# Performance work log

Measured on AMD Instinct MI355X. Metric: run time of the kernel, lower is better.

## Reference

```python
import jax, jax.numpy as jnp
import numpy as np

B, S, H = 2, 2048, 1024
N, DK = 16, 64          # heads, key/value dim (N*DK == H)
DF = 4096               # FFN hidden
SCALE = 1.0 / float(DK) ** 0.5
EPS = 1e-5


def _layer_norm(x, g, b):
    mu = jnp.mean(x, axis=-1, keepdims=True)
    var = jnp.var(x, axis=-1, keepdims=True)
    return (x - mu) * jax.lax.rsqrt(var + EPS) * g + b


def setup_inputs() -> dict:
    key = jax.random.key(0)
    ks = jax.random.split(key, 12)
    s = 0.02
    return {
        "x": jax.random.normal(ks[0], (B, S, H), dtype=jnp.float32),
        "Wq": jax.random.normal(ks[1], (N * DK, H), dtype=jnp.float32) * s,
        "bq": jnp.zeros((N * DK,), jnp.float32),
        "Wk": jax.random.normal(ks[2], (N * DK, H), dtype=jnp.float32) * s,
        "bk": jnp.zeros((N * DK,), jnp.float32),
        "Wv": jax.random.normal(ks[3], (N * DK, H), dtype=jnp.float32) * s,
        "bv": jnp.zeros((N * DK,), jnp.float32),
        "Wo": jax.random.normal(ks[4], (H, N * DK), dtype=jnp.float32) * s,
        "bo": jnp.zeros((H,), jnp.float32),
        "W1": jax.random.normal(ks[5], (DF, H), dtype=jnp.float32) * s,
        "b1": jnp.zeros((DF,), jnp.float32),
        "W2": jax.random.normal(ks[6], (H, DF), dtype=jnp.float32) * s,
        "b2": jnp.zeros((H,), jnp.float32),
        "ln1_g": jnp.ones((H,), jnp.float32),
        "ln1_b": jnp.zeros((H,), jnp.float32),
        "ln2_g": jnp.ones((H,), jnp.float32),
        "ln2_b": jnp.zeros((H,), jnp.float32),
    }


def _mha(x, Wq, bq, Wk, bk, Wv, bv, Wo, bo):
    b = x.shape[0]
    q = (x @ Wq.T + bq).reshape(b, -1, N, DK)  # [B,T,N,DK]
    k = (x @ Wk.T + bk).reshape(b, -1, N, DK)
    v = (x @ Wv.T + bv).reshape(b, -1, N, DK)
    # naive full-score attention, faithful to torch einsum layout
    scores = jnp.einsum('btnd,bsnd->tsbn', q, k) * SCALE  # [T,S,B,N]
    p = jax.nn.softmax(scores, axis=1)                    # softmax over S (dim=1)
    attn = jnp.einsum('tsbn,bsnd->btnd', p, v)            # [B,T,N,DK]
    attn = attn.reshape(b, attn.shape[1], -1)             # [B,T,N*DK]
    return attn @ Wo.T + bo


def reference(x, Wq, bq, Wk, bk, Wv, bv, Wo, bo, W1, b1, W2, b2,
              ln1_g, ln1_b, ln2_g, ln2_b):
    # post-LN encoder layer: x = LN(x + MHA(x)); x = LN(x + FFN(x))
    h = _layer_norm(x + _mha(x, Wq, bq, Wk, bk, Wv, bv, Wo, bo), ln1_g, ln1_b)
    ff = jax.nn.relu(h @ W1.T + b1) @ W2.T + b2
    return _layer_norm(h + ff, ln2_g, ln2_b)
```

## Files before the change

kernel.cpp:

```cpp
#include <hip/hip_runtime.h>
#include <stdint.h>


typedef unsigned short u16;
typedef __bf16 bf16x8 __attribute__((ext_vector_type(8)));
typedef float  f32x4  __attribute__((ext_vector_type(4)));

__device__ __forceinline__ u16 f2bf(float f) {
    unsigned int u = __float_as_uint(f);
    u += 0x7FFFu + ((u >> 16) & 1u);
    return (u16)(u >> 16);
}

__device__ __forceinline__ float bf2f(u16 v) {
    return __uint_as_float((unsigned)v << 16);
}

__device__ __forceinline__ unsigned pack_bf16_hi(float lo, float hi) {
#if __has_builtin(__builtin_amdgcn_perm)
    return __builtin_amdgcn_perm(__float_as_uint(hi), __float_as_uint(lo), 0x07060302u);
#else
    return (__float_as_uint(lo) >> 16) | (__float_as_uint(hi) & 0xFFFF0000u);
#endif
}

__device__ __forceinline__ void async_load16(const u16* g, u16* l) {
    __builtin_amdgcn_global_load_lds(
        (__attribute__((address_space(1))) void*)g,
        (__attribute__((address_space(3))) void*)l, 16, 0, 0);
}

struct CvtArgs {
    const float* src[7];
    u16*         dst[7];
    int          n[7];
};

__global__ __launch_bounds__(256) void k_cvt_all(CvtArgs a) {
    const int seg = blockIdx.y;
    const int i = (blockIdx.x * 256 + threadIdx.x) * 8;
    if (i >= a.n[seg]) return;
    const float* in = a.src[seg];
    u16* out = a.dst[seg];
    float4 x = *(const float4*)(in + i);
    float4 y = *(const float4*)(in + i + 4);
    uint4 o;
    o.x = (unsigned)f2bf(x.x) | ((unsigned)f2bf(x.y) << 16);
    o.y = (unsigned)f2bf(x.z) | ((unsigned)f2bf(x.w) << 16);
    o.z = (unsigned)f2bf(y.x) | ((unsigned)f2bf(y.y) << 16);
    o.w = (unsigned)f2bf(y.z) | ((unsigned)f2bf(y.w) << 16);
    *(uint4*)(out + i) = o;
}

__global__ __launch_bounds__(256) void k_concat3(const float* __restrict__ a,
                                                 const float* __restrict__ b,
                                                 const float* __restrict__ c,
                                                 float* __restrict__ out) {
    int i = blockIdx.x * 256 + threadIdx.x;
    if (i >= 3072) return;
    out[i] = (i < 1024) ? a[i] : (i < 2048 ? b[i - 1024] : c[i - 2048]);
}

template<int OUT_BF16, int RELU>
__global__ __launch_bounds__(256, 4) void k_gemm_bt(
    const u16* __restrict__ A, const u16* __restrict__ Bw,
    const float* __restrict__ bias, void* __restrict__ Y,
    int M, int N, int K)
{
    __shared__ u16 As[128 * 32];
    __shared__ u16 Bs[128 * 32];
    const int tid  = threadIdx.x;
    const int wave = tid >> 6, lane = tid & 63;
    const int lm = lane & 15, lq = lane >> 4;
    const int m0 = blockIdx.x * 128, n0 = blockIdx.y * 128;
    const int wr = (wave >> 1) * 64, wc = (wave & 1) * 64;

    const int ksz = K / gridDim.z;
    const int ks  = blockIdx.z * ksz, ke = ks + ksz;

    const size_t arow = (size_t)(m0 + (lane >> 2)) * K + (lane & 3) * 8;
    const size_t brow = (size_t)(n0 + (lane >> 2)) * K + (lane & 3) * 8;
    const int c0 = wave * 2, c1 = wave * 2 + 1;

    f32x4 acc[4][4];
#pragma unroll
    for (int i = 0; i < 4; i++)
#pragma unroll
        for (int j = 0; j < 4; j++) acc[i][j] = (f32x4){0.f, 0.f, 0.f, 0.f};

    for (int k0 = ks; k0 < ke; k0 += 32) {
        __syncthreads();
        async_load16(A  + arow + (size_t)(c0 * 16) * K + k0, As + c0 * 512);
        async_load16(A  + arow + (size_t)(c1 * 16) * K + k0, As + c1 * 512);
        async_load16(Bw + brow + (size_t)(c0 * 16) * K + k0, Bs + c0 * 512);
        async_load16(Bw + brow + (size_t)(c1 * 16) * K + k0, Bs + c1 * 512);
        __syncthreads();

        bf16x8 af[4], bf[4];
#pragma unroll
        for (int i = 0; i < 4; i++)
            af[i] = *(const bf16x8*)(As + (wr + i * 16 + lm) * 32 + lq * 8);
#pragma unroll
        for (int j = 0; j < 4; j++)
            bf[j] = *(const bf16x8*)(Bs + (wc + j * 16 + lm) * 32 + lq * 8);
#pragma unroll
        for (int i = 0; i < 4; i++)
#pragma unroll
            for (int j = 0; j < 4; j++)
                acc[i][j] = __builtin_amdgcn_mfma_f32_16x16x32_bf16(af[i], bf[j], acc[i][j], 0, 0, 0);
    }

    const float bsc = (blockIdx.z == 0) ? 1.f : 0.f;
    const size_t zoff = (size_t)blockIdx.z * M * N;
#pragma unroll
    for (int i = 0; i < 4; i++) {
        const int mg = m0 + wr + i * 16 + lq * 4;
#pragma unroll
        for (int j = 0; j < 4; j++) {
            const int ng = n0 + wc + j * 16 + lm;
            const float bv = bias[ng] * bsc;
#pragma unroll
            for (int r = 0; r < 4; r++) {
                float v = acc[i][j][r] + bv;
                if (RELU) v = fmaxf(v, 0.f);
                if (OUT_BF16) ((u16*)Y)[zoff + (size_t)(mg + r) * N + ng] = f2bf(v);
                else          ((float*)Y)[zoff + (size_t)(mg + r) * N + ng] = v;
            }
        }
    }
}

__global__ __launch_bounds__(256) void k_transpose_v(const u16* __restrict__ qkv,
                                                     u16* __restrict__ vt) {
    __shared__ u16 T[64 * 72];
    const int tid = threadIdx.x;
    const int t0 = blockIdx.x * 64;
    const int bn = blockIdx.y;
    const int b = bn >> 4, n = bn & 15;
    {
        const int r = tid >> 2, c = (tid & 3) * 16;
        const u16* src = qkv + (size_t)(b * 2048 + t0 + r) * 3072 + 2048 + n * 64 + c;
        *(uint4*)&T[r * 72 + c]     = *(const uint4*)(src);
        *(uint4*)&T[r * 72 + c + 8] = *(const uint4*)(src + 8);
    }
    __syncthreads();
    {
        const int d = tid >> 2, c = (tid & 3) * 16;
        union { u16 h[16]; uint4 v[2]; } tmp;
#pragma unroll
        for (int j = 0; j < 16; j++) {
            const int w = c + j;
            const int k = ((w & 3) << 4) + (w >> 2);
            tmp.h[j] = T[k * 72 + d];
        }
        u16* dst = vt + (size_t)(bn * 64 + d) * 2048 + t0 + c;
        *(uint4*)(dst)     = tmp.v[0];
        *(uint4*)(dst + 8) = tmp.v[1];
    }
}

__global__ __launch_bounds__(256, 2) void k_flash(const u16* __restrict__ qkv,
                                                  const u16* __restrict__ vt,
                                                  u16* __restrict__ attn) {
    __shared__ u16 Ks[64 * 72];
    __shared__ u16 Vs[64 * 72];
    __shared__ u16 Ps[4 * 32 * 72];
    const int tid = threadIdx.x, wave = tid >> 6, lane = tid & 63;
    const int lm = lane & 15, lq = lane >> 4;
    const int b = blockIdx.z, n = blockIdx.y, qt0 = blockIdx.x * 128;

    bf16x8 qf[2][2];
#pragma unroll
    for (int mh = 0; mh < 2; mh++) {
        const u16* qp = qkv + (size_t)(b * 2048 + qt0 + wave * 32 + mh * 16 + lm) * 3072
                        + n * 64 + lq * 8;
        const bf16x8 q0r = *(const bf16x8*)(qp);
        const bf16x8 q1r = *(const bf16x8*)(qp + 32);
#pragma unroll
        for (int j = 0; j < 8; j++) {
            qf[mh][0][j] = (__bf16)((float)q0r[j] * 0.18033688f);
            qf[mh][1][j] = (__bf16)((float)q1r[j] * 0.18033688f);
        }
    }

    float lsum[2][4];
    f32x4 oacc[2][4];
#pragma unroll
    for (int mh = 0; mh < 2; mh++)
#pragma unroll
        for (int r = 0; r < 4; r++) { lsum[mh][r] = 0.f; }
#pragma unroll
    for (int mh = 0; mh < 2; mh++)
#pragma unroll
        for (int dt = 0; dt < 4; dt++) oacc[mh][dt] = (f32x4){0.f, 0.f, 0.f, 0.f};

    const int sr = tid >> 2, sc = (tid & 3) * 16;
    const u16* kg = qkv + (size_t)(b * 2048 + sr) * 3072 + 1024 + n * 64 + sc;
    const u16* vg = vt + (size_t)((b * 16 + n) * 64 + sr) * 2048 + sc;
    u16* PsW = Ps + wave * 32 * 72;

    uint4 kr0 = *(const uint4*)(kg);
    uint4 kr1 = *(const uint4*)(kg + 8);
    uint4 vr0 = *(const uint4*)(vg);
    uint4 vr1 = *(const uint4*)(vg + 8);

    for (int kt = 0; kt < 2048; kt += 64) {
        __syncthreads();
        *(uint4*)&Ks[sr * 72 + sc]     = kr0;
        *(uint4*)&Ks[sr * 72 + sc + 8] = kr1;
        *(uint4*)&Vs[sr * 72 + sc]     = vr0;
        *(uint4*)&Vs[sr * 72 + sc + 8] = vr1;
        __syncthreads();

        if (kt + 64 < 2048) {
            kr0 = *(const uint4*)(kg + (size_t)(kt + 64) * 3072);
            kr1 = *(const uint4*)(kg + (size_t)(kt + 64) * 3072 + 8);
            vr0 = *(const uint4*)(vg + kt + 64);
            vr1 = *(const uint4*)(vg + kt + 64 + 8);
        }

        f32x4 sf[2][4];
#pragma unroll
        for (int nt = 0; nt < 4; nt++) {
            const bf16x8 kf0 = *(const bf16x8*)(Ks + (nt * 16 + lm) * 72 + lq * 8);
            const bf16x8 kf1 = *(const bf16x8*)(Ks + (nt * 16 + lm) * 72 + lq * 8 + 32);
#pragma unroll
            for (int mh = 0; mh < 2; mh++) {
                f32x4 z = (f32x4){0.f, 0.f, 0.f, 0.f};
                z = __builtin_amdgcn_mfma_f32_16x16x32_bf16(qf[mh][0], kf0, z, 0, 0, 0);
                z = __builtin_amdgcn_mfma_f32_16x16x32_bf16(qf[mh][1], kf1, z, 0, 0, 0);
                sf[mh][nt] = z;
            }
        }

#pragma unroll
        for (int mh = 0; mh < 2; mh++)
#pragma unroll
            for (int r = 0; r < 4; r++) {
                const float p0 = __builtin_amdgcn_exp2f(sf[mh][0][r]);
                const float p1 = __builtin_amdgcn_exp2f(sf[mh][1][r]);
                const float p2 = __builtin_amdgcn_exp2f(sf[mh][2][r]);
                const float p3 = __builtin_amdgcn_exp2f(sf[mh][3][r]);
                lsum[mh][r] += (p0 + p1) + (p2 + p3);
                uint2 w;
                w.x = pack_bf16_hi(p0, p1);
                w.y = pack_bf16_hi(p2, p3);
                *(uint2*)&PsW[(mh * 16 + lq * 4 + r) * 72 + lm * 4] = w;
            }

#pragma unroll
        for (int s2 = 0; s2 < 2; s2++) {
            bf16x8 pf[2];
#pragma unroll
            for (int mh = 0; mh < 2; mh++)
                pf[mh] = *(const bf16x8*)(PsW + (mh * 16 + lm) * 72 + s2 * 32 + lq * 8);
#pragma unroll
            for (int dt = 0; dt < 4; dt++) {
                const bf16x8 vf = *(const bf16x8*)(Vs + (dt * 16 + lm) * 72 + s2 * 32 + lq * 8);
#pragma unroll
                for (int mh = 0; mh < 2; mh++)
                    oacc[mh][dt] = __builtin_amdgcn_mfma_f32_16x16x32_bf16(pf[mh], vf, oacc[mh][dt], 0, 0, 0);
            }
        }
    }

#pragma unroll
    for (int mh = 0; mh < 2; mh++)
#pragma unroll
        for (int r = 0; r < 4; r++) {
#pragma unroll
            for (int off = 8; off >= 1; off >>= 1)
                lsum[mh][r] += __shfl_xor(lsum[mh][r], off, 16);
            lsum[mh][r] = 1.f / lsum[mh][r];
        }
#pragma unroll
    for (int mh = 0; mh < 2; mh++)
#pragma unroll
        for (int dt = 0; dt < 4; dt++)
#pragma unroll
            for (int r = 0; r < 4; r++) {
                const float o = oacc[mh][dt][r] * lsum[mh][r];
                attn[(size_t)(b * 2048 + qt0 + wave * 32 + mh * 16 + lq * 4 + r) * 1024
                     + n * 64 + dt * 16 + lm] = f2bf(o);
            }
}

template<int WRITE_BF16>
__global__ __launch_bounds__(256) void k_ln_p4(const float* __restrict__ a,
                                               const u16* __restrict__ pb,
                                               const float* __restrict__ g,
                                               const float* __restrict__ be,
                                               float* __restrict__ outf,
                                               u16* __restrict__ outb) {
    const int row = blockIdx.x, tid = threadIdx.x;
    const size_t base = (size_t)row * 1024 + tid * 4;
    const float4 av = *(const float4*)(a + base);
    float x0 = av.x, x1 = av.y, x2 = av.z, x3 = av.w;
#pragma unroll
    for (int z = 0; z < 4; z++) {
        const uint2 w = *(const uint2*)(pb + (size_t)z * 4096 * 1024 + base);
        x0 += __uint_as_float(w.x << 16);
        x1 += __uint_as_float(w.x & 0xFFFF0000u);
        x2 += __uint_as_float(w.y << 16);
        x3 += __uint_as_float(w.y & 0xFFFF0000u);
    }
    float s1 = x0 + x1 + x2 + x3;
    float s2 = x0 * x0 + x1 * x1 + x2 * x2 + x3 * x3;
#pragma unroll
    for (int off = 32; off >= 1; off >>= 1) {
        s1 += __shfl_down(s1, off);
        s2 += __shfl_down(s2, off);
    }
    __shared__ float red[8];
    __shared__ float stats[2];
    const int wave = tid >> 6, lane = tid & 63;
    if (lane == 0) { red[wave] = s1; red[4 + wave] = s2; }
    __syncthreads();
    if (tid == 0) {
        const float t1 = red[0] + red[1] + red[2] + red[3];
        const float t2 = red[4] + red[5] + red[6] + red[7];
        const float mean = t1 * (1.f / 1024.f);
        const float var = t2 * (1.f / 1024.f) - mean * mean;
        stats[0] = mean;
        stats[1] = rsqrtf(var + 1e-5f);
    }
    __syncthreads();
    const float mean = stats[0], rstd = stats[1];
    const int c = tid * 4;
    const float4 gv = *(const float4*)(g + c);
    const float4 bev = *(const float4*)(be + c);
    float4 y;
    y.x = (x0 - mean) * rstd * gv.x + bev.x;
    y.y = (x1 - mean) * rstd * gv.y + bev.y;
    y.z = (x2 - mean) * rstd * gv.z + bev.z;
    y.w = (x3 - mean) * rstd * gv.w + bev.w;
    *(float4*)(outf + base) = y;
    if (WRITE_BF16) {
        uint2 o;
        o.x = (unsigned)f2bf(y.x) | ((unsigned)f2bf(y.y) << 16);
        o.y = (unsigned)f2bf(y.z) | ((unsigned)f2bf(y.w) << 16);
        *(uint2*)(outb + base) = o;
    }
}

extern "C" void kernel_launch(void* const* d_in, const int* in_sizes, int n_in,
                              void* d_out, int out_size, void* d_ws, size_t ws_size,
                              hipStream_t stream) {
    const float* x   = (const float*)d_in[0];
    const float* Wq  = (const float*)d_in[1];
    const float* bq  = (const float*)d_in[2];
    const float* Wk  = (const float*)d_in[3];
    const float* bk  = (const float*)d_in[4];
    const float* Wv  = (const float*)d_in[5];
    const float* bv  = (const float*)d_in[6];
    const float* Wo  = (const float*)d_in[7];
    const float* bo  = (const float*)d_in[8];
    const float* W1  = (const float*)d_in[9];
    const float* b1  = (const float*)d_in[10];
    const float* W2  = (const float*)d_in[11];
    const float* b2  = (const float*)d_in[12];
    const float* g1  = (const float*)d_in[13];
    const float* be1 = (const float*)d_in[14];
    const float* g2  = (const float*)d_in[15];
    const float* be2 = (const float*)d_in[16];

    char* ws = (char*)d_ws;
    const size_t MB = 1024 * 1024;
    u16*   wqkv = (u16*)(ws + 0);
    u16*   wo_b = (u16*)(ws + 6 * MB);
    u16*   w1_b = (u16*)(ws + 8 * MB);
    u16*   w2_b = (u16*)(ws + 16 * MB);
    float* bqkv = (float*)(ws + 24 * MB);
    u16*   xb   = (u16*)(ws + 25 * MB);
    u16*   qkv  = (u16*)(ws + 33 * MB);
    u16*   vt   = (u16*)(ws + 57 * MB);
    u16*   attn = (u16*)(ws + 65 * MB);
    u16*   op4  = (u16*)(ws + 33 * MB);
    float* h    = (float*)(ws + 65 * MB);
    u16*   hb   = (u16*)(ws + 81 * MB);
    u16*   ff1  = (u16*)(ws + 33 * MB);
    u16*   fp4  = (u16*)(ws + 81 * MB);

    CvtArgs ca;
    ca.src[0] = x;  ca.dst[0] = xb;                  ca.n[0] = 4096 * 1024;
    ca.src[1] = Wq; ca.dst[1] = wqkv;                ca.n[1] = 1024 * 1024;
    ca.src[2] = Wk; ca.dst[2] = wqkv + 1024 * 1024;  ca.n[2] = 1024 * 1024;
    ca.src[3] = Wv; ca.dst[3] = wqkv + 2 * 1024 * 1024; ca.n[3] = 1024 * 1024;
    ca.src[4] = Wo; ca.dst[4] = wo_b;                ca.n[4] = 1024 * 1024;
    ca.src[5] = W1; ca.dst[5] = w1_b;                ca.n[5] = 4096 * 1024;
    ca.src[6] = W2; ca.dst[6] = w2_b;                ca.n[6] = 4096 * 1024;
    k_cvt_all<<<dim3(2048, 7), 256, 0, stream>>>(ca);
    k_concat3<<<12, 256, 0, stream>>>(bq, bk, bv, bqkv);

    k_gemm_bt<1, 0><<<dim3(32, 24), 256, 0, stream>>>(
        xb, wqkv, bqkv, qkv, 4096, 3072, 1024);

    k_transpose_v<<<dim3(32, 32), 256, 0, stream>>>(qkv, vt);

    k_flash<<<dim3(16, 16, 2), 256, 0, stream>>>(qkv, vt, attn);

    k_gemm_bt<1, 0><<<dim3(32, 8, 4), 256, 0, stream>>>(
        attn, wo_b, bo, op4, 4096, 1024, 1024);

    k_ln_p4<1><<<4096, 256, 0, stream>>>(x, op4, g1, be1, h, hb);

    k_gemm_bt<1, 1><<<dim3(32, 32), 256, 0, stream>>>(
        hb, w1_b, b1, ff1, 4096, 4096, 1024);

    k_gemm_bt<1, 0><<<dim3(32, 8, 4), 256, 0, stream>>>(
        ff1, w2_b, b2, fp4, 4096, 1024, 4096);

    k_ln_p4<0><<<4096, 256, 0, stream>>>(h, fp4, g2, be2, (float*)d_out, nullptr);
}
```

Baseline: 343.0 us.

## Split flash attention over two KV halves and combine partials in a separate kernel

```diff
diff --git a/kernel.cpp b/kernel.cpp
--- a/kernel.cpp
+++ b/kernel.cpp
@@ -159,15 +159,18 @@
     }
 }
 
-__global__ __launch_bounds__(256, 2) void k_flash(const u16* __restrict__ qkv,
+__global__ __launch_bounds__(512, 4) void k_flash(const u16* __restrict__ qkv,
                                                   const u16* __restrict__ vt,
-                                                  u16* __restrict__ attn) {
+                                                  float* __restrict__ opart,
+                                                  float* __restrict__ lsb) {
     __shared__ u16 Ks[64 * 72];
     __shared__ u16 Vs[64 * 72];
-    __shared__ u16 Ps[4 * 32 * 72];
+    __shared__ u16 Ps[8 * 32 * 72];
     const int tid = threadIdx.x, wave = tid >> 6, lane = tid & 63;
     const int lm = lane & 15, lq = lane >> 4;
-    const int b = blockIdx.z, n = blockIdx.y, qt0 = blockIdx.x * 128;
+    const int zz = blockIdx.z;
+    const int b = zz >> 1, kvh = zz & 1;
+    const int n = blockIdx.y, qt0 = blockIdx.x * 256;
 
     bf16x8 qf[2][2];
 #pragma unroll
@@ -194,29 +197,23 @@
 #pragma unroll
         for (int dt = 0; dt < 4; dt++) oacc[mh][dt] = (f32x4){0.f, 0.f, 0.f, 0.f};
 
-    const int sr = tid >> 2, sc = (tid & 3) * 16;
-    const u16* kg = qkv + (size_t)(b * 2048 + sr) * 3072 + 1024 + n * 64 + sc;
-    const u16* vg = vt + (size_t)((b * 16 + n) * 64 + sr) * 2048 + sc;
+    const int sr = tid >> 3, sc = (tid & 7) * 8;
+    const u16* kg = qkv + (size_t)(b * 2048 + kvh * 1024 + sr) * 3072 + 1024 + n * 64 + sc;
+    const u16* vg = vt + (size_t)((b * 16 + n) * 64 + sr) * 2048 + kvh * 1024 + sc;
     u16* PsW = Ps + wave * 32 * 72;
 
-    uint4 kr0 = *(const uint4*)(kg);
-    uint4 kr1 = *(const uint4*)(kg + 8);
-    uint4 vr0 = *(const uint4*)(vg);
-    uint4 vr1 = *(const uint4*)(vg + 8);
-
-    for (int kt = 0; kt < 2048; kt += 64) {
+    uint4 kr = *(const uint4*)(kg);
+    uint4 vr = *(const uint4*)(vg);
+
+    for (int kt = 0; kt < 1024; kt += 64) {
         __syncthreads();
-        *(uint4*)&Ks[sr * 72 + sc]     = kr0;
-        *(uint4*)&Ks[sr * 72 + sc + 8] = kr1;
-        *(uint4*)&Vs[sr * 72 + sc]     = vr0;
-        *(uint4*)&Vs[sr * 72 + sc + 8] = vr1;
+        *(uint4*)&Ks[sr * 72 + sc] = kr;
+        *(uint4*)&Vs[sr * 72 + sc] = vr;
         __syncthreads();
 
-        if (kt + 64 < 2048) {
-            kr0 = *(const uint4*)(kg + (size_t)(kt + 64) * 3072);
-            kr1 = *(const uint4*)(kg + (size_t)(kt + 64) * 3072 + 8);
-            vr0 = *(const uint4*)(vg + kt + 64);
-            vr1 = *(const uint4*)(vg + kt + 64 + 8);
+        if (kt + 64 < 1024) {
+            kr = *(const uint4*)(kg + (size_t)(kt + 64) * 3072);
+            vr = *(const uint4*)(vg + kt + 64);
         }
 
         f32x4 sf[2][4];
@@ -271,18 +268,42 @@
 #pragma unroll
             for (int off = 8; off >= 1; off >>= 1)
                 lsum[mh][r] += __shfl_xor(lsum[mh][r], off, 16);
-            lsum[mh][r] = 1.f / lsum[mh][r];
-        }
+        }
+
+    const size_t half = (size_t)kvh * 4096 * 1024;
 #pragma unroll
     for (int mh = 0; mh < 2; mh++)
 #pragma unroll
         for (int dt = 0; dt < 4; dt++)
 #pragma unroll
             for (int r = 0; r < 4; r++) {
-                const float o = oacc[mh][dt][r] * lsum[mh][r];
-                attn[(size_t)(b * 2048 + qt0 + wave * 32 + mh * 16 + lq * 4 + r) * 1024
-                     + n * 64 + dt * 16 + lm] = f2bf(o);
-            }
+                opart[half + (size_t)(b * 2048 + qt0 + wave * 32 + mh * 16 + lq * 4 + r) * 1024
+                      + n * 64 + dt * 16 + lm] = oacc[mh][dt][r];
+            }
+    if (lm == 0) {
+#pragma unroll
+        for (int mh = 0; mh < 2; mh++)
+#pragma unroll
+            for (int r = 0; r < 4; r++) {
+                const int qrow = qt0 + wave * 32 + mh * 16 + lq * 4 + r;
+                lsb[(size_t)kvh * 4096 * 16 + (size_t)(b * 2048 + qrow) * 16 + n] = lsum[mh][r];
+            }
+    }
+}
+
+__global__ __launch_bounds__(256) void k_att_combine(const float* __restrict__ opart,
+                                                     const float* __restrict__ lsb,
+                                                     u16* __restrict__ attn) {
+    const int row = blockIdx.x, tid = threadIdx.x;
+    const int n = tid >> 4, d0 = (tid & 15) * 4;
+    const size_t o = (size_t)row * 1024 + n * 64 + d0;
+    const float4 a = *(const float4*)(opart + o);
+    const float4 c = *(const float4*)(opart + (size_t)4096 * 1024 + o);
+    const float inv = 1.f / (lsb[(size_t)row * 16 + n] + lsb[(size_t)4096 * 16 + row * 16 + n]);
+    uint2 w;
+    w.x = (unsigned)f2bf((a.x + c.x) * inv) | ((unsigned)f2bf((a.y + c.y) * inv) << 16);
+    w.y = (unsigned)f2bf((a.z + c.z) * inv) | ((unsigned)f2bf((a.w + c.w) * inv) << 16);
+    *(uint2*)(attn + o) = w;
 }
 
 template<int WRITE_BF16>
@@ -366,20 +387,22 @@
 
     char* ws = (char*)d_ws;
     const size_t MB = 1024 * 1024;
-    u16*   wqkv = (u16*)(ws + 0);
-    u16*   wo_b = (u16*)(ws + 6 * MB);
-    u16*   w1_b = (u16*)(ws + 8 * MB);
-    u16*   w2_b = (u16*)(ws + 16 * MB);
-    float* bqkv = (float*)(ws + 24 * MB);
-    u16*   xb   = (u16*)(ws + 25 * MB);
-    u16*   qkv  = (u16*)(ws + 33 * MB);
-    u16*   vt   = (u16*)(ws + 57 * MB);
-    u16*   attn = (u16*)(ws + 65 * MB);
-    u16*   op4  = (u16*)(ws + 33 * MB);
-    float* h    = (float*)(ws + 65 * MB);
-    u16*   hb   = (u16*)(ws + 81 * MB);
-    u16*   ff1  = (u16*)(ws + 33 * MB);
-    u16*   fp4  = (u16*)(ws + 81 * MB);
+    u16*   wqkv  = (u16*)(ws + 0);
+    u16*   wo_b  = (u16*)(ws + 6 * MB);
+    u16*   w1_b  = (u16*)(ws + 8 * MB);
+    u16*   w2_b  = (u16*)(ws + 16 * MB);
+    float* bqkv  = (float*)(ws + 24 * MB);
+    float* lsb   = (float*)(ws + 24 * MB + 512 * 1024);
+    u16*   xb    = (u16*)(ws + 25 * MB);
+    u16*   qkv   = (u16*)(ws + 33 * MB);
+    u16*   vt    = (u16*)(ws + 57 * MB);
+    float* opart = (float*)(ws + 65 * MB);
+    u16*   attn  = (u16*)(ws + 97 * MB);
+    u16*   op4   = (u16*)(ws + 33 * MB);
+    float* h     = (float*)(ws + 65 * MB);
+    u16*   hb    = (u16*)(ws + 81 * MB);
+    u16*   ff1   = (u16*)(ws + 33 * MB);
+    u16*   fp4   = (u16*)(ws + 81 * MB);
 
     CvtArgs ca;
     ca.src[0] = x;  ca.dst[0] = xb;                  ca.n[0] = 4096 * 1024;
@@ -397,7 +420,9 @@
 
     k_transpose_v<<<dim3(32, 32), 256, 0, stream>>>(qkv, vt);
 
-    k_flash<<<dim3(16, 16, 2), 256, 0, stream>>>(qkv, vt, attn);
+    k_flash<<<dim3(8, 16, 4), 512, 0, stream>>>(qkv, vt, opart, lsb);
+
+    k_att_combine<<<4096, 256, 0, stream>>>(opart, lsb, attn);
 
     k_gemm_bt<1, 0><<<dim3(32, 8, 4), 256, 0, stream>>>(
         attn, wo_b, bo, op4, 4096, 1024, 1024);
```

Measured after the change: 352.8 us. 1.03x slower.
